# Kernel tuning notes

Measured on AMD Instinct MI355X. Metric: run time of the kernel, lower is better.

The kernel has to match this reference:

```python
import jax, jax.numpy as jnp
import numpy as np

N = 100000      # nodes
E = 1_600_000   # edges per snapshot
T = 8           # timesteps / snapshots
X_DIM = 128
H = 64          # h_dim
Z = 32          # z_dim


def setup_inputs() -> dict:
    key = jax.random.key(0)
    ks = jax.random.split(key, 16)
    s = 0.05
    return {
        "x":    jax.random.normal(ks[0], (N, X_DIM), jnp.float32),
        "eis":  jax.random.randint(ks[1], (T, 2, E), 0, N, jnp.int32),
        "ews":  jax.random.uniform(ks[2], (T, E), jnp.float32),
        "W1":   jax.random.normal(ks[3], (X_DIM, H), jnp.float32) * s,
        "b1":   jnp.zeros((H,), jnp.float32),
        "W2":   jax.random.normal(ks[4], (H, H), jnp.float32) * s,
        "b2":   jnp.zeros((H,), jnp.float32),
        "Wih":  jax.random.normal(ks[5], (3 * H, H), jnp.float32) * s,
        "Whh":  jax.random.normal(ks[6], (3 * H, H), jnp.float32) * s,
        "bih":  jnp.zeros((3 * H,), jnp.float32),
        "bhh":  jnp.zeros((3 * H,), jnp.float32),
        "Wlin": jax.random.normal(ks[7], (Z, H), jnp.float32) * s,
        "blin": jnp.zeros((Z,), jnp.float32),
    }


def gcn_prop(h, ei, ew):
    # GCNConv propagation with self loops: D^{-1/2}(A+I)D^{-1/2} h
    # h: [N,F], ei: [2,E] int, ew: [E]
    n = h.shape[0]
    loops = jnp.arange(n, dtype=ei.dtype)
    src = jnp.concatenate([ei[0], loops])          # [E+N]
    dst = jnp.concatenate([ei[1], loops])
    w = jnp.concatenate([ew, jnp.ones((n,), h.dtype)])
    deg = jax.ops.segment_sum(w, dst, num_segments=n)       # [N]
    dinv = jnp.where(deg > 0, jax.lax.rsqrt(deg), 0.0)
    norm = dinv[src] * w * dinv[dst]               # [E+N]
    msg = h[src] * norm[:, None]                   # gather + scale
    return jax.ops.segment_sum(msg, dst, num_segments=n)    # scatter-add


def gru_layer(xs, Wih, Whh, bih, bhh):
    # PyTorch nn.GRU (1 layer), xs: [T, N, H_in]
    h0 = jnp.zeros((xs.shape[1], Whh.shape[1]), xs.dtype)

    def step(h, x):
        gi = x @ Wih.T + bih                        # [N,3H]
        gh = h @ Whh.T + bhh
        ir, iz, inn = jnp.split(gi, 3, axis=-1)
        hr, hz, hn = jnp.split(gh, 3, axis=-1)
        r = jax.nn.sigmoid(ir + hr)
        z = jax.nn.sigmoid(iz + hz)
        nn_ = jnp.tanh(inn + r * hn)
        h_new = (1.0 - z) * nn_ + z * h
        return h_new, h_new

    _, ys = jax.lax.scan(step, h0, xs)
    return ys


def reference(x, eis, ews, W1, b1, W2, b2, Wih, Whh, bih, bhh, Wlin, blin):
    # --- encode(): per-snapshot 2-layer GCN (eval mode: dropout/DropEdge = identity) ---
    xw1 = x @ W1                                    # shared across snapshots [N,H]

    def snapshot(ei, ew):
        h1 = jax.nn.relu(gcn_prop(xw1, ei, ew) + b1)   # GCNConv layer 1
        return gcn_prop(h1 @ W2, ei, ew) + b2          # GCNConv layer 2

    embeds = jax.vmap(snapshot)(eis, ews)           # [T,N,H]

    # --- recurrent head: tanh -> GRU -> Linear ---
    hs = gru_layer(jnp.tanh(embeds), Wih, Whh, bih, bhh)   # [T,N,H]
    return hs @ Wlin.T + blin                       # [T,N,Z]
```

## Files before the change

kernel.cpp:

```cpp
#include <hip/hip_runtime.h>
#include <math.h>

#define N_NODES 100000
#define NE      1600000
#define T_STEPS 8

__device__ __forceinline__ float sigmoid_f(float x) { return 1.f / (1.f + __expf(-x)); }
__device__ __forceinline__ float tanh_f(float x) {
  float e = __expf(2.f * x);
  return 1.f - 2.f / (e + 1.f);
}


__global__ void k_init(unsigned long long* __restrict__ pk) {
  int i = blockIdx.x * 256 + threadIdx.x;
  if (i < N_NODES) pk[i] = 0ULL;
}

__global__ void k_hist(const int* __restrict__ dst, const float* __restrict__ ew,
                       unsigned long long* __restrict__ pk) {
  int e = blockIdx.x * 256 + threadIdx.x;
  if (e < NE) {
    unsigned q = __float2uint_rn(ew[e] * 16777216.0f);
    atomicAdd(&pk[dst[e]], (1ULL << 40) | (unsigned long long)q);
  }
}

__global__ void k_scan_a(const unsigned long long* __restrict__ pk, int* __restrict__ rp,
                         int* __restrict__ sums) {
  __shared__ int sdata[256];
  int tid = threadIdx.x;
  int base = blockIdx.x * 2048 + tid * 8;
  int v[8];
  int tot = 0;
#pragma unroll
  for (int i = 0; i < 8; ++i) {
    int idx = base + i;
    int c = (idx < N_NODES) ? (int)(pk[idx] >> 40) : 0;
    v[i] = tot; tot += c;
  }
  sdata[tid] = tot;
  __syncthreads();
  for (int off = 1; off < 256; off <<= 1) {
    int x = (tid >= off) ? sdata[tid - off] : 0;
    __syncthreads();
    sdata[tid] += x;
    __syncthreads();
  }
  int texcl = sdata[tid] - tot;
  if (tid == 255) sums[blockIdx.x] = sdata[255];
#pragma unroll
  for (int i = 0; i < 8; ++i) {
    int idx = base + i;
    if (idx < N_NODES) rp[idx] = texcl + v[i];
  }
}

__global__ void k_scan_c(int* __restrict__ rp, const int* __restrict__ sums, int* __restrict__ cur,
                         unsigned long long* __restrict__ pk, float* __restrict__ degv) {
  __shared__ int sbase;
  int tid = threadIdx.x;
  int cid = blockIdx.x >> 3;
  if (tid == 0) {
    int b = 0;
    for (int c = 0; c < cid; ++c) b += sums[c];
    sbase = b;
  }
  __syncthreads();
  int idx = blockIdx.x * 256 + tid;
  if (idx < N_NODES) {
    int vv = rp[idx] + sbase;
    rp[idx] = vv;
    cur[idx] = vv;
    float deg = 1.0f + (float)(pk[idx] & 0xFFFFFFFFFFULL) * 5.9604644775390625e-08f;
    degv[idx] = rsqrtf(deg);
    pk[idx] = 0ULL;
  }
  if (blockIdx.x == 0 && tid == 0) rp[N_NODES] = NE;
}

__global__ void k_place(const int* __restrict__ src, const int* __restrict__ dst,
                        const float* __restrict__ ew, const float* __restrict__ dinv,
                        int* __restrict__ cur, int2* __restrict__ pairs) {
  int e = blockIdx.x * 256 + threadIdx.x;
  if (e < NE) {
    int s = src[e], d = dst[e];
    float w = ew[e];
    int p = atomicAdd(&cur[d], 1);
    pairs[p] = make_int2(s, __float_as_int(dinv[s] * w * dinv[d]));
  }
}


__global__ void k_prop(const float* __restrict__ hin, const int* __restrict__ rp,
                       const int2* __restrict__ pairs, const float* __restrict__ dinv,
                       const float* __restrict__ bias, float* __restrict__ hout,
                       int mode ) {
  int node = __builtin_amdgcn_readfirstlane(blockIdx.x * 4 + (threadIdx.x >> 6));
  int lane = threadIdx.x & 63;
  int half = lane >> 5;
  int fl   = lane & 31;
  const float2* hin2 = (const float2*)hin;

  float di = dinv[node];
  float2 selfv = hin2[(size_t)node * 32 + fl];
  int e0 = rp[node], e1 = rp[node + 1];

  float2 a0 = make_float2(0.f, 0.f), a1 = a0, a2 = a0, a3 = a0;
  int j = e0;
  for (; j + 8 <= e1; j += 8) {
    int2 p0 = pairs[j + half];
    int2 p1 = pairs[j + 2 + half];
    int2 p2 = pairs[j + 4 + half];
    int2 p3 = pairs[j + 6 + half];
    float2 h0 = hin2[(size_t)p0.x * 32 + fl];
    float2 h1 = hin2[(size_t)p1.x * 32 + fl];
    float2 h2 = hin2[(size_t)p2.x * 32 + fl];
    float2 h3 = hin2[(size_t)p3.x * 32 + fl];
    float w0 = __int_as_float(p0.y), w1 = __int_as_float(p1.y);
    float w2 = __int_as_float(p2.y), w3 = __int_as_float(p3.y);
    a0.x = fmaf(h0.x, w0, a0.x); a0.y = fmaf(h0.y, w0, a0.y);
    a1.x = fmaf(h1.x, w1, a1.x); a1.y = fmaf(h1.y, w1, a1.y);
    a2.x = fmaf(h2.x, w2, a2.x); a2.y = fmaf(h2.y, w2, a2.y);
    a3.x = fmaf(h3.x, w3, a3.x); a3.y = fmaf(h3.y, w3, a3.y);
  }
  for (; j < e1; j += 2) {
    int jj = j + half;
    int idx = (jj < e1) ? jj : (e1 - 1);
    int2 p = pairs[idx];
    float w = (jj < e1) ? __int_as_float(p.y) : 0.f;
    float2 hv = hin2[(size_t)p.x * 32 + fl];
    a0.x = fmaf(hv.x, w, a0.x); a0.y = fmaf(hv.y, w, a0.y);
  }

  float accx = (a0.x + a1.x) + (a2.x + a3.x);
  float accy = (a0.y + a1.y) + (a2.y + a3.y);
  float ox = __shfl(accx, fl + 32);
  float oy = __shfl(accy, fl + 32);
  if (half == 0) {
    float2 bv = *(const float2*)&bias[2 * fl];
    float sx = accx + ox + selfv.x * di * di + bv.x;
    float sy = accy + oy + selfv.y * di * di + bv.y;
    float2 o;
    o.x = (mode == 0) ? fmaxf(sx, 0.f) : tanh_f(sx);
    o.y = (mode == 0) ? fmaxf(sy, 0.f) : tanh_f(sy);
    *(float2*)&hout[(size_t)node * 64 + 2 * fl] = o;
  }
}


__global__ void k_xw1(const float* __restrict__ x, const float* __restrict__ W1, float* __restrict__ o) {
  __shared__ float sW[128 * 64];
  __shared__ float sx[32 * 128];
  int tid = threadIdx.x;
  int row0 = blockIdx.x * 32;
  for (int i = tid; i < 128 * 64; i += 256) sW[i] = W1[i];
  for (int i = tid; i < 32 * 128; i += 256) {
    int r = i >> 7, c = i & 127;
    sx[i] = x[(size_t)(row0 + r) * 128 + c];
  }
  __syncthreads();
  int f = tid & 63, w = tid >> 6;
  float acc[8];
#pragma unroll
  for (int m = 0; m < 8; ++m) acc[m] = 0.f;
  for (int k = 0; k < 128; ++k) {
    float wv = sW[k * 64 + f];
#pragma unroll
    for (int m = 0; m < 8; ++m)
      acc[m] = fmaf(sx[(w * 8 + m) * 128 + k], wv, acc[m]);
  }
#pragma unroll
  for (int m = 0; m < 8; ++m)
    o[(size_t)(row0 + w * 8 + m) * 64 + f] = acc[m];
}

__global__ void k_mm64(float* __restrict__ a, const float* __restrict__ W2) {
  __shared__ float sW[64 * 64];
  __shared__ float sx[32 * 64];
  int tid = threadIdx.x;
  int row0 = blockIdx.x * 32;
  for (int i = tid; i < 64 * 64; i += 256) sW[i] = W2[i];
  for (int i = tid; i < 32 * 64; i += 256) {
    int r = i >> 6, c = i & 63;
    sx[i] = a[(size_t)(row0 + r) * 64 + c];
  }
  __syncthreads();
  int f = tid & 63, w = tid >> 6;
  float acc[8];
#pragma unroll
  for (int m = 0; m < 8; ++m) acc[m] = 0.f;
  for (int k = 0; k < 64; ++k) {
    float wv = sW[k * 64 + f];
#pragma unroll
    for (int m = 0; m < 8; ++m)
      acc[m] = fmaf(sx[(w * 8 + m) * 64 + k], wv, acc[m]);
  }
#pragma unroll
  for (int m = 0; m < 8; ++m)
    a[(size_t)(row0 + w * 8 + m) * 64 + f] = acc[m];
}

__global__ void k_prep(const float* __restrict__ Wih, const float* __restrict__ Whh,
                       const float* __restrict__ Wlin, float* __restrict__ Pih,
                       float* __restrict__ Phh, float* __restrict__ WlinT) {
  int i = blockIdx.x * 256 + threadIdx.x;
  int k = i >> 8, c = i & 255, f = c >> 2, g = c & 3;
  float vi = 0.f, vh = 0.f;
  if (g < 3) {
    vi = Wih[(size_t)(g * 64 + f) * 64 + k];
    vh = Whh[(size_t)(g * 64 + f) * 64 + k];
  }
  Pih[i] = vi;
  Phh[i] = vh;
  if (i < 2048) {
    int kk = i >> 5, j = i & 31;
    WlinT[i] = Wlin[(size_t)j * 64 + kk];
  }
}

__global__ __launch_bounds__(256, 3) void k_gru(
    const float* __restrict__ gt, float* __restrict__ h,
    const float* __restrict__ Pih, const float* __restrict__ Phh,
    const float* __restrict__ bih, const float* __restrict__ bhh,
    const float* __restrict__ WlinT, const float* __restrict__ blin,
    float* __restrict__ outt, int first) {
  __shared__ float sWi[8 * 256];
  __shared__ float sWh[8 * 256];
  __shared__ float sx[32 * 64];
  __shared__ float sh[32 * 64];

  int tid = threadIdx.x;
  int node0 = blockIdx.x * 32;

  {
    const float4* gx = (const float4*)(gt + (size_t)node0 * 64);
    float4* lx = (float4*)sx;
    float4* lh = (float4*)sh;
    lx[tid] = gx[tid];
    lx[tid + 256] = gx[tid + 256];
    if (first) {
      float4 z4 = make_float4(0.f, 0.f, 0.f, 0.f);
      lh[tid] = z4;
      lh[tid + 256] = z4;
    } else {
      const float4* gh = (const float4*)(h + (size_t)node0 * 64);
      lh[tid] = gh[tid];
      lh[tid + 256] = gh[tid + 256];
    }
  }

  int f = tid & 63;
  int w = tid >> 6;
  int mb = w * 8;

  float air[8], aiz[8], ain[8], ahr[8], ahz[8], ahn[8];
#pragma unroll
  for (int m = 0; m < 8; ++m) { air[m]=0.f; aiz[m]=0.f; ain[m]=0.f; ahr[m]=0.f; ahz[m]=0.f; ahn[m]=0.f; }

  for (int kt = 0; kt < 64; kt += 8) {
    __syncthreads();
    {
      const float4* gi = (const float4*)(Pih + (size_t)kt * 256);
      const float4* gh4 = (const float4*)(Phh + (size_t)kt * 256);
      float4* li = (float4*)sWi;
      float4* lh4 = (float4*)sWh;
      li[tid] = gi[tid];
      li[tid + 256] = gi[tid + 256];
      lh4[tid] = gh4[tid];
      lh4[tid + 256] = gh4[tid + 256];
    }
    __syncthreads();
#pragma unroll
    for (int kg = 0; kg < 8; kg += 4) {
      float4 wi0 = *reinterpret_cast<const float4*>(&sWi[(kg + 0) * 256 + f * 4]);
      float4 wi1 = *reinterpret_cast<const float4*>(&sWi[(kg + 1) * 256 + f * 4]);
      float4 wi2 = *reinterpret_cast<const float4*>(&sWi[(kg + 2) * 256 + f * 4]);
      float4 wi3 = *reinterpret_cast<const float4*>(&sWi[(kg + 3) * 256 + f * 4]);
      float4 wh0 = *reinterpret_cast<const float4*>(&sWh[(kg + 0) * 256 + f * 4]);
      float4 wh1 = *reinterpret_cast<const float4*>(&sWh[(kg + 1) * 256 + f * 4]);
      float4 wh2 = *reinterpret_cast<const float4*>(&sWh[(kg + 2) * 256 + f * 4]);
      float4 wh3 = *reinterpret_cast<const float4*>(&sWh[(kg + 3) * 256 + f * 4]);
#pragma unroll
      for (int m = 0; m < 8; ++m) {
        float4 xm = *reinterpret_cast<const float4*>(&sx[(mb + m) * 64 + kt + kg]);
        float4 hm = *reinterpret_cast<const float4*>(&sh[(mb + m) * 64 + kt + kg]);
        air[m] = fmaf(xm.x, wi0.x, air[m]); aiz[m] = fmaf(xm.x, wi0.y, aiz[m]); ain[m] = fmaf(xm.x, wi0.z, ain[m]);
        ahr[m] = fmaf(hm.x, wh0.x, ahr[m]); ahz[m] = fmaf(hm.x, wh0.y, ahz[m]); ahn[m] = fmaf(hm.x, wh0.z, ahn[m]);
        air[m] = fmaf(xm.y, wi1.x, air[m]); aiz[m] = fmaf(xm.y, wi1.y, aiz[m]); ain[m] = fmaf(xm.y, wi1.z, ain[m]);
        ahr[m] = fmaf(hm.y, wh1.x, ahr[m]); ahz[m] = fmaf(hm.y, wh1.y, ahz[m]); ahn[m] = fmaf(hm.y, wh1.z, ahn[m]);
        air[m] = fmaf(xm.z, wi2.x, air[m]); aiz[m] = fmaf(xm.z, wi2.y, aiz[m]); ain[m] = fmaf(xm.z, wi2.z, ain[m]);
        ahr[m] = fmaf(hm.z, wh2.x, ahr[m]); ahz[m] = fmaf(hm.z, wh2.y, ahz[m]); ahn[m] = fmaf(hm.z, wh2.z, ahn[m]);
        air[m] = fmaf(xm.w, wi3.x, air[m]); aiz[m] = fmaf(xm.w, wi3.y, aiz[m]); ain[m] = fmaf(xm.w, wi3.z, ain[m]);
        ahr[m] = fmaf(hm.w, wh3.x, ahr[m]); ahz[m] = fmaf(hm.w, wh3.y, ahz[m]); ahn[m] = fmaf(hm.w, wh3.z, ahn[m]);
      }
    }
  }

  float bir = bih[f], biz = bih[64 + f], bin = bih[128 + f];
  float bhr = bhh[f], bhz = bhh[64 + f], bhn = bhh[128 + f];

  float hnew[8];
#pragma unroll
  for (int m = 0; m < 8; ++m) {
    float r = sigmoid_f(air[m] + bir + ahr[m] + bhr);
    float z = sigmoid_f(aiz[m] + biz + ahz[m] + bhz);
    float nn = tanh_f(ain[m] + bin + r * (ahn[m] + bhn));
    float hold = sh[(mb + m) * 64 + f];
    hnew[m] = (1.f - z) * nn + z * hold;
  }
#pragma unroll
  for (int m = 0; m < 8; ++m) {
    sh[(mb + m) * 64 + f] = hnew[m];
    h[(size_t)(node0 + mb + m) * 64 + f] = hnew[m];
  }

  __syncthreads();
  for (int i = tid; i < 2048; i += 256) sWi[i] = WlinT[i];
  __syncthreads();

  int j = f & 31, hi = f >> 5;
  float o0 = blin[j], o1 = o0, o2 = o0, o3 = o0;
  for (int k = 0; k < 64; ++k) {
    float wv = sWi[k * 32 + j];
    o0 = fmaf(sh[(mb + 0 + hi) * 64 + k], wv, o0);
    o1 = fmaf(sh[(mb + 2 + hi) * 64 + k], wv, o1);
    o2 = fmaf(sh[(mb + 4 + hi) * 64 + k], wv, o2);
    o3 = fmaf(sh[(mb + 6 + hi) * 64 + k], wv, o3);
  }
  outt[(size_t)(node0 + mb + 0 + hi) * 32 + j] = o0;
  outt[(size_t)(node0 + mb + 2 + hi) * 32 + j] = o1;
  outt[(size_t)(node0 + mb + 4 + hi) * 32 + j] = o2;
  outt[(size_t)(node0 + mb + 6 + hi) * 32 + j] = o3;
}


extern "C" void kernel_launch(void* const* d_in, const int* in_sizes, int n_in,
                              void* d_out, int out_size, void* d_ws, size_t ws_size,
                              hipStream_t stream) {
  const float* x    = (const float*)d_in[0];
  const int*   eis  = (const int*)d_in[1];
  const float* ews  = (const float*)d_in[2];
  const float* W1   = (const float*)d_in[3];
  const float* b1   = (const float*)d_in[4];
  const float* W2   = (const float*)d_in[5];
  const float* b2   = (const float*)d_in[6];
  const float* Wih  = (const float*)d_in[7];
  const float* Whh  = (const float*)d_in[8];
  const float* bih  = (const float*)d_in[9];
  const float* bhh  = (const float*)d_in[10];
  const float* Wlin = (const float*)d_in[11];
  const float* blin = (const float*)d_in[12];
  float* out = (float*)d_out;

  char* ws = (char*)d_ws;
  size_t off = 0;
  auto alloc = [&](size_t bytes) { char* p = ws + off; off += (bytes + 255) & ~size_t(255); return p; };
  float* xw1  = (float*)alloc((size_t)N_NODES * 64 * 4);
  float* bufA = (float*)alloc((size_t)N_NODES * 64 * 4);
  float* bufB = (float*)alloc((size_t)N_NODES * 64 * 4);
  float* hst  = (float*)alloc((size_t)N_NODES * 64 * 4);
  float* degv = (float*)alloc((size_t)N_NODES * 4);
  unsigned long long* pk = (unsigned long long*)alloc((size_t)N_NODES * 8);
  int*   rp   = (int*)alloc((size_t)(N_NODES + 1) * 4);
  int*   cur  = (int*)alloc((size_t)(N_NODES + 1) * 4);
  int*   sums = (int*)alloc(64 * 4);
  int2*  pairs = (int2*)alloc((size_t)NE * 8);
  float* Pih  = (float*)alloc(64 * 256 * 4);
  float* Phh  = (float*)alloc(64 * 256 * 4);
  float* WlinT = (float*)alloc(64 * 32 * 4);
  if (ws_size < off) return;

  const int GB_N   = (N_NODES + 255) / 256;
  const int GB_E   = (NE + 255) / 256;
  const int GB_SC  = (N_NODES + 2047) / 2048;
  const int GB_MM  = N_NODES / 32;
  const int GB_PR  = N_NODES / 4;
  const int GB_GRU = N_NODES / 32;

  k_prep<<<64, 256, 0, stream>>>(Wih, Whh, Wlin, Pih, Phh, WlinT);
  k_xw1<<<GB_MM, 256, 0, stream>>>(x, W1, xw1);
  k_init<<<GB_N, 256, 0, stream>>>(pk);

  for (int t = 0; t < T_STEPS; ++t) {
    const int* srcp = eis + (size_t)t * 2 * NE;
    const int* dstp = srcp + NE;
    const float* ewp = ews + (size_t)t * NE;

    k_hist<<<GB_E, 256, 0, stream>>>(dstp, ewp, pk);
    k_scan_a<<<GB_SC, 256, 0, stream>>>(pk, rp, sums);
    k_scan_c<<<GB_N, 256, 0, stream>>>(rp, sums, cur, pk, degv);
    k_place<<<GB_E, 256, 0, stream>>>(srcp, dstp, ewp, degv, cur, pairs);

    k_prop<<<GB_PR, 256, 0, stream>>>(xw1, rp, pairs, degv, b1, bufA, 0);
    k_mm64<<<GB_MM, 256, 0, stream>>>(bufA, W2);
    k_prop<<<GB_PR, 256, 0, stream>>>(bufA, rp, pairs, degv, b2, bufB, 1);
    k_gru<<<GB_GRU, 256, 0, stream>>>(bufB, hst, Pih, Phh, bih, bhh, WlinT, blin,
                                      out + (size_t)t * N_NODES * 32, t == 0 ? 1 : 0);
  }
}
```

Measured before the change: 3.700 ms.

## Batch degree histogram and scans across all snapshots; use readlane broadcast in GRU

```diff
diff --git a/kernel.cpp b/kernel.cpp
--- a/kernel.cpp
+++ b/kernel.cpp
@@ -14,30 +14,35 @@
 
 __global__ void k_init(unsigned long long* __restrict__ pk) {
   int i = blockIdx.x * 256 + threadIdx.x;
-  if (i < N_NODES) pk[i] = 0ULL;
-}
-
-__global__ void k_hist(const int* __restrict__ dst, const float* __restrict__ ew,
+  if (i < 8 * N_NODES) pk[i] = 0ULL;
+}
+
+__global__ void k_hist(const int* __restrict__ eis, const float* __restrict__ ews,
                        unsigned long long* __restrict__ pk) {
-  int e = blockIdx.x * 256 + threadIdx.x;
-  if (e < NE) {
-    unsigned q = __float2uint_rn(ew[e] * 16777216.0f);
-    atomicAdd(&pk[dst[e]], (1ULL << 40) | (unsigned long long)q);
-  }
-}
-
-__global__ void k_scan_a(const unsigned long long* __restrict__ pk, int* __restrict__ rp,
-                         int* __restrict__ sums) {
+  int t = blockIdx.x / 6250;
+  int e = (blockIdx.x % 6250) * 256 + threadIdx.x;
+  int d = eis[(size_t)t * 2 * NE + NE + e];
+  float w = ews[(size_t)t * NE + e];
+  unsigned q = __float2uint_rn(w * 16777216.0f);
+  atomicAdd(&pk[(size_t)t * N_NODES + d], (1ULL << 40) | (unsigned long long)q);
+}
+
+__global__ void k_scan_a(const unsigned long long* __restrict__ pkA, int* __restrict__ rpA,
+                         int* __restrict__ sumsA) {
   __shared__ int sdata[256];
+  int t = blockIdx.x / 49, c = blockIdx.x % 49;
+  const unsigned long long* pk = pkA + (size_t)t * N_NODES;
+  int* rp = rpA + (size_t)t * (N_NODES + 1);
+  int* sums = sumsA + t * 64;
   int tid = threadIdx.x;
-  int base = blockIdx.x * 2048 + tid * 8;
+  int base = c * 2048 + tid * 8;
   int v[8];
   int tot = 0;
 #pragma unroll
   for (int i = 0; i < 8; ++i) {
     int idx = base + i;
-    int c = (idx < N_NODES) ? (int)(pk[idx] >> 40) : 0;
-    v[i] = tot; tot += c;
+    int cc = (idx < N_NODES) ? (int)(pk[idx] >> 40) : 0;
+    v[i] = tot; tot += cc;
   }
   sdata[tid] = tot;
   __syncthreads();
@@ -48,7 +53,7 @@
     __syncthreads();
   }
   int texcl = sdata[tid] - tot;
-  if (tid == 255) sums[blockIdx.x] = sdata[255];
+  if (tid == 255) sums[c] = sdata[255];
 #pragma unroll
   for (int i = 0; i < 8; ++i) {
     int idx = base + i;
@@ -56,27 +61,33 @@
   }
 }
 
-__global__ void k_scan_c(int* __restrict__ rp, const int* __restrict__ sums, int* __restrict__ cur,
-                         unsigned long long* __restrict__ pk, float* __restrict__ degv) {
+__global__ void k_scan_c(int* __restrict__ rpA, const int* __restrict__ sumsA,
+                         int* __restrict__ curA, const unsigned long long* __restrict__ pkA,
+                         float* __restrict__ degvA) {
   __shared__ int sbase;
+  int t = blockIdx.x / 391, b = blockIdx.x % 391;
+  int* rp = rpA + (size_t)t * (N_NODES + 1);
+  const int* sums = sumsA + t * 64;
+  int* cur = curA + (size_t)t * N_NODES;
+  const unsigned long long* pk = pkA + (size_t)t * N_NODES;
+  float* degv = degvA + (size_t)t * N_NODES;
   int tid = threadIdx.x;
-  int cid = blockIdx.x >> 3;
+  int cid = b >> 3;
   if (tid == 0) {
-    int b = 0;
-    for (int c = 0; c < cid; ++c) b += sums[c];
-    sbase = b;
-  }
-  __syncthreads();
-  int idx = blockIdx.x * 256 + tid;
+    int bb = 0;
+    for (int c = 0; c < cid; ++c) bb += sums[c];
+    sbase = bb;
+  }
+  __syncthreads();
+  int idx = b * 256 + tid;
   if (idx < N_NODES) {
     int vv = rp[idx] + sbase;
     rp[idx] = vv;
     cur[idx] = vv;
     float deg = 1.0f + (float)(pk[idx] & 0xFFFFFFFFFFULL) * 5.9604644775390625e-08f;
     degv[idx] = rsqrtf(deg);
-    pk[idx] = 0ULL;
-  }
-  if (blockIdx.x == 0 && tid == 0) rp[N_NODES] = NE;
+  }
+  if (b == 0 && tid == 0) rp[N_NODES] = NE;
 }
 
 __global__ void k_place(const int* __restrict__ src, const int* __restrict__ dst,
@@ -227,18 +238,13 @@
     float* __restrict__ outt, int first) {
   __shared__ float sWi[8 * 256];
   __shared__ float sWh[8 * 256];
-  __shared__ float sx[32 * 64];
   __shared__ float sh[32 * 64];
 
   int tid = threadIdx.x;
   int node0 = blockIdx.x * 32;
 
   {
-    const float4* gx = (const float4*)(gt + (size_t)node0 * 64);
-    float4* lx = (float4*)sx;
     float4* lh = (float4*)sh;
-    lx[tid] = gx[tid];
-    lx[tid + 256] = gx[tid + 256];
     if (first) {
       float4 z4 = make_float4(0.f, 0.f, 0.f, 0.f);
       lh[tid] = z4;
@@ -253,6 +259,27 @@
   int f = tid & 63;
   int w = tid >> 6;
   int mb = w * 8;
+
+  int cl = f & 7;
+  int nl = mb + (f >> 3);
+  float xr[8], hr[8];
+  {
+    const float* xrow = gt + (size_t)(node0 + nl) * 64 + cl * 8;
+    float4 xa = *(const float4*)xrow;
+    float4 xb = *(const float4*)(xrow + 4);
+    xr[0]=xa.x; xr[1]=xa.y; xr[2]=xa.z; xr[3]=xa.w;
+    xr[4]=xb.x; xr[5]=xb.y; xr[6]=xb.z; xr[7]=xb.w;
+    if (first) {
+#pragma unroll
+      for (int i = 0; i < 8; ++i) hr[i] = 0.f;
+    } else {
+      const float* hrow = h + (size_t)(node0 + nl) * 64 + cl * 8;
+      float4 ha = *(const float4*)hrow;
+      float4 hb = *(const float4*)(hrow + 4);
+      hr[0]=ha.x; hr[1]=ha.y; hr[2]=ha.z; hr[3]=ha.w;
+      hr[4]=hb.x; hr[5]=hb.y; hr[6]=hb.z; hr[7]=hb.w;
+    }
+  }
 
   float air[8], aiz[8], ain[8], ahr[8], ahz[8], ahn[8];
 #pragma unroll
@@ -271,28 +298,17 @@
       lh4[tid + 256] = gh4[tid + 256];
     }
     __syncthreads();
-#pragma unroll
-    for (int kg = 0; kg < 8; kg += 4) {
-      float4 wi0 = *reinterpret_cast<const float4*>(&sWi[(kg + 0) * 256 + f * 4]);
-      float4 wi1 = *reinterpret_cast<const float4*>(&sWi[(kg + 1) * 256 + f * 4]);
-      float4 wi2 = *reinterpret_cast<const float4*>(&sWi[(kg + 2) * 256 + f * 4]);
-      float4 wi3 = *reinterpret_cast<const float4*>(&sWi[(kg + 3) * 256 + f * 4]);
-      float4 wh0 = *reinterpret_cast<const float4*>(&sWh[(kg + 0) * 256 + f * 4]);
-      float4 wh1 = *reinterpret_cast<const float4*>(&sWh[(kg + 1) * 256 + f * 4]);
-      float4 wh2 = *reinterpret_cast<const float4*>(&sWh[(kg + 2) * 256 + f * 4]);
-      float4 wh3 = *reinterpret_cast<const float4*>(&sWh[(kg + 3) * 256 + f * 4]);
+    int srcl = kt >> 3;
+#pragma unroll
+    for (int kk = 0; kk < 8; ++kk) {
+      float4 wi = *reinterpret_cast<const float4*>(&sWi[kk * 256 + f * 4]);
+      float4 wh = *reinterpret_cast<const float4*>(&sWh[kk * 256 + f * 4]);
 #pragma unroll
       for (int m = 0; m < 8; ++m) {
-        float4 xm = *reinterpret_cast<const float4*>(&sx[(mb + m) * 64 + kt + kg]);
-        float4 hm = *reinterpret_cast<const float4*>(&sh[(mb + m) * 64 + kt + kg]);
-        air[m] = fmaf(xm.x, wi0.x, air[m]); aiz[m] = fmaf(xm.x, wi0.y, aiz[m]); ain[m] = fmaf(xm.x, wi0.z, ain[m]);
-        ahr[m] = fmaf(hm.x, wh0.x, ahr[m]); ahz[m] = fmaf(hm.x, wh0.y, ahz[m]); ahn[m] = fmaf(hm.x, wh0.z, ahn[m]);
-        air[m] = fmaf(xm.y, wi1.x, air[m]); aiz[m] = fmaf(xm.y, wi1.y, aiz[m]); ain[m] = fmaf(xm.y, wi1.z, ain[m]);
-        ahr[m] = fmaf(hm.y, wh1.x, ahr[m]); ahz[m] = fmaf(hm.y, wh1.y, ahz[m]); ahn[m] = fmaf(hm.y, wh1.z, ahn[m]);
-        air[m] = fmaf(xm.z, wi2.x, air[m]); aiz[m] = fmaf(xm.z, wi2.y, aiz[m]); ain[m] = fmaf(xm.z, wi2.z, ain[m]);
-        ahr[m] = fmaf(hm.z, wh2.x, ahr[m]); ahz[m] = fmaf(hm.z, wh2.y, ahz[m]); ahn[m] = fmaf(hm.z, wh2.z, ahn[m]);
-        air[m] = fmaf(xm.w, wi3.x, air[m]); aiz[m] = fmaf(xm.w, wi3.y, aiz[m]); ain[m] = fmaf(xm.w, wi3.z, ain[m]);
-        ahr[m] = fmaf(hm.w, wh3.x, ahr[m]); ahz[m] = fmaf(hm.w, wh3.y, ahz[m]); ahn[m] = fmaf(hm.w, wh3.z, ahn[m]);
+        float xs = __int_as_float(__builtin_amdgcn_readlane(__float_as_int(xr[kk]), m * 8 + srcl));
+        float hs = __int_as_float(__builtin_amdgcn_readlane(__float_as_int(hr[kk]), m * 8 + srcl));
+        air[m] = fmaf(xs, wi.x, air[m]); aiz[m] = fmaf(xs, wi.y, aiz[m]); ain[m] = fmaf(xs, wi.z, ain[m]);
+        ahr[m] = fmaf(hs, wh.x, ahr[m]); ahz[m] = fmaf(hs, wh.y, ahz[m]); ahn[m] = fmaf(hs, wh.z, ahn[m]);
       }
     }
   }
@@ -360,41 +376,42 @@
   float* bufA = (float*)alloc((size_t)N_NODES * 64 * 4);
   float* bufB = (float*)alloc((size_t)N_NODES * 64 * 4);
   float* hst  = (float*)alloc((size_t)N_NODES * 64 * 4);
-  float* degv = (float*)alloc((size_t)N_NODES * 4);
-  unsigned long long* pk = (unsigned long long*)alloc((size_t)N_NODES * 8);
-  int*   rp   = (int*)alloc((size_t)(N_NODES + 1) * 4);
-  int*   cur  = (int*)alloc((size_t)(N_NODES + 1) * 4);
-  int*   sums = (int*)alloc(64 * 4);
+  float* degv = (float*)alloc((size_t)8 * N_NODES * 4);
+  unsigned long long* pk = (unsigned long long*)alloc((size_t)8 * N_NODES * 8);
+  int*   rp   = (int*)alloc((size_t)8 * (N_NODES + 1) * 4);
+  int*   cur  = (int*)alloc((size_t)8 * N_NODES * 4);
+  int*   sums = (int*)alloc(8 * 64 * 4);
   int2*  pairs = (int2*)alloc((size_t)NE * 8);
   float* Pih  = (float*)alloc(64 * 256 * 4);
   float* Phh  = (float*)alloc(64 * 256 * 4);
   float* WlinT = (float*)alloc(64 * 32 * 4);
   if (ws_size < off) return;
 
-  const int GB_N   = (N_NODES + 255) / 256;
-  const int GB_E   = (NE + 255) / 256;
-  const int GB_SC  = (N_NODES + 2047) / 2048;
+  const int GB_E   = NE / 256;
   const int GB_MM  = N_NODES / 32;
   const int GB_PR  = N_NODES / 4;
   const int GB_GRU = N_NODES / 32;
 
   k_prep<<<64, 256, 0, stream>>>(Wih, Whh, Wlin, Pih, Phh, WlinT);
   k_xw1<<<GB_MM, 256, 0, stream>>>(x, W1, xw1);
-  k_init<<<GB_N, 256, 0, stream>>>(pk);
+
+  k_init<<<(8 * N_NODES + 255) / 256, 256, 0, stream>>>(pk);
+  k_hist<<<8 * GB_E, 256, 0, stream>>>(eis, ews, pk);
+  k_scan_a<<<8 * 49, 256, 0, stream>>>(pk, rp, sums);
+  k_scan_c<<<8 * 391, 256, 0, stream>>>(rp, sums, cur, pk, degv);
 
   for (int t = 0; t < T_STEPS; ++t) {
     const int* srcp = eis + (size_t)t * 2 * NE;
     const int* dstp = srcp + NE;
     const float* ewp = ews + (size_t)t * NE;
-
-    k_hist<<<GB_E, 256, 0, stream>>>(dstp, ewp, pk);
-    k_scan_a<<<GB_SC, 256, 0, stream>>>(pk, rp, sums);
-    k_scan_c<<<GB_N, 256, 0, stream>>>(rp, sums, cur, pk, degv);
-    k_place<<<GB_E, 256, 0, stream>>>(srcp, dstp, ewp, degv, cur, pairs);
-
-    k_prop<<<GB_PR, 256, 0, stream>>>(xw1, rp, pairs, degv, b1, bufA, 0);
+    const int* rpt = rp + (size_t)t * (N_NODES + 1);
+    float* dvt = degv + (size_t)t * N_NODES;
+
+    k_place<<<GB_E, 256, 0, stream>>>(srcp, dstp, ewp, dvt, cur + (size_t)t * N_NODES, pairs);
+
+    k_prop<<<GB_PR, 256, 0, stream>>>(xw1, rpt, pairs, dvt, b1, bufA, 0);
     k_mm64<<<GB_MM, 256, 0, stream>>>(bufA, W2);
-    k_prop<<<GB_PR, 256, 0, stream>>>(bufA, rp, pairs, degv, b2, bufB, 1);
+    k_prop<<<GB_PR, 256, 0, stream>>>(bufA, rpt, pairs, dvt, b2, bufB, 1);
     k_gru<<<GB_GRU, 256, 0, stream>>>(bufB, hst, Pih, Phh, bih, bhh, WlinT, blin,
                                       out + (size_t)t * N_NODES * 32, t == 0 ? 1 : 0);
   }
```

After: 3.745 ms. No clear change (+1.2%).
